# Optimization experiments

Hardware: AMD Instinct MI355X
Metric: run time of the kernel (lower is better)

The kernel has to match this reference:

```python
import jax, jax.numpy as jnp
import numpy as np

D = 128      # dim_hidden
L = 8        # topological levels (level 0 = primary inputs)
M = 32768    # nodes per level
N = L * M
G = 5        # gate types: maj/not/and/or/xor -> 5 param sets
F = 2        # fan-in per gate node


def setup_inputs() -> dict:
    key = jax.random.key(0)
    ks = jax.random.split(key, 18)
    p = lambda k, sh: jax.random.normal(k, sh, jnp.float32) * 0.05
    return {
        's': jax.random.normal(ks[0], (N, D), jnp.float32),
        't': jax.random.normal(ks[1], (N, D), jnp.float32),
        'gate': jax.random.randint(ks[2], (N,), 0, G, jnp.int32),
        'fanin': jax.random.randint(ks[3], (L - 1, M, F), 0, M, jnp.int32),
        'hs_W': p(ks[4], (2 * D, D)), 'hs_b': p(ks[5], (D,)),
        'aggr_W1': p(ks[6], (G, 2 * D, D)), 'aggr_b1': p(ks[7], (G, D)),
        'aggr_W2': p(ks[8], (G, D, D)), 'aggr_b2': p(ks[9], (G, D)),
        'aggr_W3': p(ks[10], (G, D, D)), 'aggr_b3': p(ks[11], (G, D)),
        'gru_Wi': p(ks[12], (G, D, 3 * D)), 'gru_Wh': p(ks[13], (G, D, 3 * D)),
        'gru_bi': p(ks[14], (G, 3 * D)), 'gru_bh': p(ks[15], (G, 3 * D)),
    }


def _forward(s, t, gate, fanin, hs_W, hs_b, aggr_W1, aggr_b1, aggr_W2, aggr_b2,
             aggr_W3, aggr_b3, gru_Wi, gru_Wh, gru_bi, gru_bh):
    hs = jnp.concatenate([s, t], -1) @ hs_W + hs_b          # [N,D]
    hf = jnp.zeros((N, D), hs.dtype)                        # functional state, zero-init
    for lvl in range(1, L):                                 # level-synchronous sweep
        lo = lvl * M
        g_l = gate[lo:lo + M]                               # [M] gate type of dst nodes
        oh = jax.nn.one_hot(g_l, G, dtype=hs.dtype)         # [M,G] gate selector
        src = (lvl - 1) * M + fanin[lvl - 1]                # [M,F] global fan-in indices
        src_state = jnp.concatenate([hs[src], hf[src]], -1)  # [M,F,2D] node_state gather
        # per-gate-type edge MLP (TFMlpAggr): 3-layer MLP on source states, sum over fan-in
        h1 = jax.nn.relu(jnp.einsum('mfc,gcd->gmfd', src_state, aggr_W1) + aggr_b1[:, None, None, :])
        h2 = jax.nn.relu(jnp.einsum('gmfd,gde->gmfe', h1, aggr_W2) + aggr_b2[:, None, None, :])
        m = jnp.einsum('gmfe,gek->gmfk', h2, aggr_W3) + aggr_b3[:, None, None, :]
        msg = jnp.einsum('gmd,mg->md', m.sum(axis=2), oh)   # [M,D] select own gate's aggr
        # per-gate-type GRU update of hf (torch GRU math, seq_len=1)
        h = hf[lo:lo + M]                                   # [M,D]
        gi = jnp.einsum('md,gdk->gmk', msg, gru_Wi) + gru_bi[:, None, :]  # [G,M,3D]
        gh = jnp.einsum('md,gdk->gmk', h, gru_Wh) + gru_bh[:, None, :]
        r = jax.nn.sigmoid(gi[..., :D] + gh[..., :D])
        z = jax.nn.sigmoid(gi[..., D:2 * D] + gh[..., D:2 * D])
        n = jnp.tanh(gi[..., 2 * D:] + r * gh[..., 2 * D:])
        h_new = jnp.einsum('gmd,mg->md', (1.0 - z) * n + z * h[None], oh)
        hf = hf.at[lo:lo + M].set(h_new)                    # scatter-write back
    return hs, hf


def reference(s, t, gate, fanin, hs_W, hs_b, aggr_W1, aggr_b1, aggr_W2, aggr_b2,
              aggr_W3, aggr_b3, gru_Wi, gru_Wh, gru_bi, gru_bh):
    return _forward(s, t, gate, fanin, hs_W, hs_b, aggr_W1, aggr_b1, aggr_W2,
                    aggr_b2, aggr_W3, aggr_b3, gru_Wi, gru_Wh, gru_bi, gru_bh)
```

## Files before the change

### kernel.cpp

```cpp
#include <hip/hip_runtime.h>
#include <hip/hip_bf16.h>

#define DD 128
#define LL 8
#define MM 32768
#define NN (LL*MM)
#define GG 5
#define FF 2
#define SORT_STRIDE 33408

typedef __attribute__((ext_vector_type(8))) short short8;
typedef __attribute__((ext_vector_type(4))) short short4v;
typedef __attribute__((ext_vector_type(4))) float f32x4;

#define MFMA16(a,b,c) __builtin_amdgcn_mfma_f32_16x16x32_bf16((a),(b),(c),0,0,0)

__device__ __forceinline__ short f2bf(float x){
  __hip_bfloat16 h = __float2bfloat16(x);
  return *reinterpret_cast<short*>(&h);
}

__device__ __forceinline__ short8 pack8(f32x4 a, f32x4 b){
  short8 r;
  r[0]=f2bf(a[0]); r[1]=f2bf(a[1]); r[2]=f2bf(a[2]); r[3]=f2bf(a[3]);
  r[4]=f2bf(b[0]); r[5]=f2bf(b[1]); r[6]=f2bf(b[2]); r[7]=f2bf(b[3]);
  return r;
}

__global__ void prep_kernel(const float* __restrict__ hs_W, const float* __restrict__ W1,
                            const float* __restrict__ W2, const float* __restrict__ W3,
                            const float* __restrict__ Wi,
                            short* __restrict__ hsWt, short* __restrict__ W1t,
                            short* __restrict__ W2t, short* __restrict__ W3t,
                            short* __restrict__ Wit, int* __restrict__ cntcur)
{
  if (blockIdx.x == 0 && threadIdx.x < 70) cntcur[threadIdx.x] = 0;
  int u = blockIdx.x*256 + threadIdx.x;
  const float* src; short* dst; int ldw;
  if (u < 4096){
    int i=u, ct=i>>9, kc=(i>>6)&7, ln=i&63;
    src = hs_W + (size_t)(kc*32 + 8*(ln>>4))*128 + ct*16 + (ln&15);
    dst = hsWt + (size_t)i*8; ldw=128;
  } else if (u < 24576){
    int v=u-4096, g=v>>12, i=v&4095, ct=i>>9, kc=(i>>6)&7, ln=i&63;
    src = W1 + (size_t)g*32768 + (size_t)(kc*32 + 8*(ln>>4))*128 + ct*16 + (ln&15);
    dst = W1t + (size_t)g*32768 + i*8; ldw=128;
  } else if (u < 34816){
    int v=u-24576, g=v>>11, i=v&2047, ct=i>>8, kc=(i>>6)&3, ln=i&63;
    src = W2 + (size_t)g*16384 + (size_t)(kc*32 + 8*(ln>>4))*128 + ct*16 + (ln&15);
    dst = W2t + (size_t)g*16384 + i*8; ldw=128;
  } else if (u < 45056){
    int v=u-34816, g=v>>11, i=v&2047, ct=i>>8, kc=(i>>6)&3, ln=i&63;
    src = W3 + (size_t)g*16384 + (size_t)(kc*32 + 8*(ln>>4))*128 + ct*16 + (ln&15);
    dst = W3t + (size_t)g*16384 + i*8; ldw=128;
  } else {
    int v=u-45056, g=v/6144, i=v%6144, ct=i>>8, kc=(i>>6)&3, ln=i&63;
    src = Wi + (size_t)g*49152 + (size_t)(kc*32 + 8*(ln>>4))*384 + ct*16 + (ln&15);
    dst = Wit + (size_t)g*49152 + i*8; ldw=384;
  }
  short8 o;
#pragma unroll
  for (int j=0;j<8;++j) o[j] = f2bf(src[(size_t)j*ldw]);
  *(short8*)dst = o;
}

__global__ void count_kernel(const int* __restrict__ gate, int* __restrict__ cnt){
  __shared__ int lc[GG];
  const int li = blockIdx.x >> 7;
  const int m  = ((blockIdx.x & 127) << 8) + threadIdx.x;
  if (threadIdx.x < GG) lc[threadIdx.x] = 0;
  __syncthreads();
  int g = gate[(li+1)*MM + m];
  atomicAdd(&lc[g], 1);
  __syncthreads();
  if (threadIdx.x < GG && lc[threadIdx.x] > 0)
    atomicAdd(&cnt[li*GG + threadIdx.x], lc[threadIdx.x]);
}

__global__ void offs_kernel(const int* __restrict__ cnt, int* __restrict__ off,
                            int* __restrict__ pend, int* __restrict__ sorted){
  __shared__ int se[35], sp[35];
  const int tid = threadIdx.x;
  if (tid < LL-1){
    int l = tid, o = 0;
    for (int g = 0; g < GG; ++g){
      off[l*GG+g] = o;
      int c = cnt[l*GG+g];
      pend[l*GG+g] = o + c;
      se[l*GG+g] = o + c;
      o += ((c + 31) >> 5) << 5;
      sp[l*GG+g] = o;
    }
  }
  __syncthreads();
  for (int b = 0; b < 35; ++b){
    int l = b / GG;
    for (int i = se[b] + tid; i < sp[b]; i += 256)
      sorted[l*SORT_STRIDE + i] = -1;
  }
}

__global__ void scatter_kernel(const int* __restrict__ gate, const int* __restrict__ off,
                               int* __restrict__ cur, int* __restrict__ sorted){
  __shared__ int lc[GG];
  __shared__ int base[GG];
  const int li = blockIdx.x >> 7;
  const int m  = ((blockIdx.x & 127) << 8) + threadIdx.x;
  if (threadIdx.x < GG) lc[threadIdx.x] = 0;
  __syncthreads();
  int g = gate[(li+1)*MM + m];
  int p = atomicAdd(&lc[g], 1);
  __syncthreads();
  if (threadIdx.x < GG)
    base[threadIdx.x] = atomicAdd(&cur[li*GG + threadIdx.x], lc[threadIdx.x]);
  __syncthreads();
  sorted[li*SORT_STRIDE + off[li*GG+g] + base[g] + p] = m;
}

__global__ __launch_bounds__(256,3) void hs_kernel(
    const float* __restrict__ s, const float* __restrict__ t,
    const short* __restrict__ Wt, const float* __restrict__ b,
    float* __restrict__ hs, short* __restrict__ hs_sh,
    float* __restrict__ hf, short* __restrict__ hf_sh)
{
  __shared__ __align__(16) short Xs[16384];
  const int tid=threadIdx.x, lane=tid&63, w=tid>>6;
  const int l15=lane&15, lq=lane>>4;
  const int row0 = blockIdx.x*64;

  {
    const int r = tid>>2, p = tid&3;
    const float* srow = s + (size_t)(row0+r)*DD;
    const float* trow = t + (size_t)(row0+r)*DD;
    const int rf = r>>4, rl = r&15;
    f32x4 va[16];
#pragma unroll
    for (int i=0;i<8;++i){
      int u = p + 4*i;
      const float* pp = (u<16) ? (srow + 8*u) : (trow + 8*(u-16));
      va[2*i]   = *(const f32x4*)pp;
      va[2*i+1] = *(const f32x4*)(pp+4);
    }
#pragma unroll
    for (int i=0;i<8;++i){
      int u = p + 4*i;
      short8 v = pack8(va[2*i], va[2*i+1]);
      *(short8*)(Xs + ((rf*8+(u>>2))*64 + (u&3)*16 + rl)*8) = v;
    }
  }

  if (row0 < MM){
    f32x4 zf4 = {0.f,0.f,0.f,0.f};
    short8 zs8 = {0,0,0,0,0,0,0,0};
    const size_t basei = (size_t)row0*DD;
    for (int i=tid; i<2048; i+=256) *(f32x4*)(hf + basei + i*4) = zf4;
    for (int i=tid; i<1024; i+=256) *(short8*)(hf_sh + basei + i*8) = zs8;
  }
  __syncthreads();

  f32x4 zf = {0.f,0.f,0.f,0.f};
  const short* Aw = Wt + (16*w)*512 + lane*8;
  short8 af[16];
#pragma unroll
  for (int i=0;i<16;++i) af[i] = *(const short8*)(Aw + i*512);

  f32x4 acc[4][2];
#pragma unroll
  for (int rr=0;rr<4;++rr){ acc[rr][0]=zf; acc[rr][1]=zf; }
#pragma unroll
  for (int kc=0;kc<8;++kc){
    short8 bx[4];
#pragma unroll
    for (int rr=0;rr<4;++rr)
      bx[rr] = *(const short8*)(Xs + ((rr*8 + kc)*64 + lane)*8);
#pragma unroll
    for (int rr=0;rr<4;++rr){
      acc[rr][0] = MFMA16(af[kc],   bx[rr], acc[rr][0]);
      acc[rr][1] = MFMA16(af[8+kc], bx[rr], acc[rr][1]);
    }
  }

  f32x4 bv0 = *(const f32x4*)(b + 32*w + 4*lq);
  f32x4 bv1 = *(const f32x4*)(b + 32*w + 16 + 4*lq);
#pragma unroll
  for (int rr=0;rr<4;++rr){
    int row = row0 + rr*16 + l15;
#pragma unroll
    for (int q=0;q<2;++q){
      f32x4 bv = q ? bv1 : bv0;
      int col = 32*w + 16*q + 4*lq;
      f32x4 o; short4v pk;
#pragma unroll
      for (int j=0;j<4;++j){ o[j] = acc[rr][q][j] + bv[j]; pk[j] = f2bf(o[j]); }
      *(f32x4*)(hs + (size_t)row*DD + col) = o;
      *(short4v*)(hs_sh + (size_t)row*DD + col) = pk;
    }
  }
}

__global__ __launch_bounds__(256,3) void level_kernel(
    int lvl, float* __restrict__ hfg,
    const short* __restrict__ hs_sh, short* __restrict__ hf_sh,
    const int* __restrict__ fanin,
    const short* __restrict__ W1t, const short* __restrict__ W2t,
    const short* __restrict__ W3t, const short* __restrict__ Wit,
    const float* __restrict__ b1, const float* __restrict__ b2,
    const float* __restrict__ b3, const float* __restrict__ bi,
    const float* __restrict__ bh,
    const int* __restrict__ off, const int* __restrict__ pend,
    const int* __restrict__ sorted)
{
  __shared__ __align__(16) short Xs[16384];
  __shared__ int nodebuf[32];
  __shared__ int srcbuf[64];
  __shared__ int ginfo;

  const int tid=threadIdx.x, lane=tid&63, w=tid>>6;
  const int l15=lane&15, lq=lane>>4;
  const int li = lvl-1;
  const int pos0 = blockIdx.x*32;

  if (tid==0){
    int g=-1;
    for (int q=0;q<GG;++q)
      if (pos0>=off[li*GG+q] && pos0<pend[li*GG+q]){ g=q; break; }
    ginfo=g;
  }
  if (tid<32) nodebuf[tid] = sorted[li*SORT_STRIDE + pos0 + tid];
  if (tid<64){
    int mg = sorted[li*SORT_STRIDE + pos0 + (tid>>1)];
    srcbuf[tid] = (mg>=0) ? li*MM + fanin[((size_t)li*MM+mg)*FF + (tid&1)] : 0;
  }
  __syncthreads();
  const int g = ginfo;
  if (g<0) return;

  {
    const int r = tid>>2, p = tid&3;
    const int src = srcbuf[r];
    const short* hsrow = hs_sh + (size_t)src*DD;
    const short* hfrow = hf_sh + (size_t)src*DD;
    const int rf = r>>4, rl = r&15;
    short8 va[8];
#pragma unroll
    for (int i=0;i<8;++i){
      int u = p + 4*i;
      va[i] = *(const short8*)((u<16) ? (hsrow + 8*u) : (hfrow + 8*(u-16)));
    }
#pragma unroll
    for (int i=0;i<8;++i){
      int u = p + 4*i;
      *(short8*)(Xs + ((rf*8+(u>>2))*64 + (u&3)*16 + rl)*8) = va[i];
    }
  }
  __syncthreads();

  f32x4 zf = {0.f,0.f,0.f,0.f};

  f32x4 acc[4][2];
#pragma unroll
  for (int rr=0;rr<4;++rr){ acc[rr][0]=zf; acc[rr][1]=zf; }
  {
    const short* A1w = W1t + (size_t)g*32768 + (16*w)*512 + lane*8;
    short8 af[16];
#pragma unroll
    for (int i=0;i<16;++i) af[i] = *(const short8*)(A1w + i*512);
#pragma unroll
    for (int kc=0;kc<8;++kc){
      short8 bx[4];
#pragma unroll
      for (int rr=0;rr<4;++rr)
        bx[rr] = *(const short8*)(Xs + ((rr*8 + kc)*64 + lane)*8);
#pragma unroll
      for (int rr=0;rr<4;++rr){
        acc[rr][0] = MFMA16(af[kc],   bx[rr], acc[rr][0]);
        acc[rr][1] = MFMA16(af[8+kc], bx[rr], acc[rr][1]);
      }
    }
  }
  __syncthreads();
  {
    f32x4 bv0 = *(const f32x4*)(b1 + g*DD + 32*w + 4*lq);
    f32x4 bv1 = *(const f32x4*)(b1 + g*DD + 32*w + 16 + 4*lq);
#pragma unroll
    for (int rr=0;rr<4;++rr){
#pragma unroll
      for (int q=0;q<2;++q){
        f32x4 bv = q ? bv1 : bv0;
        short4v pk;
#pragma unroll
        for (int j=0;j<4;++j) pk[j] = f2bf(fmaxf(acc[rr][q][j] + bv[j], 0.f));
        *(short4v*)(Xs + ((rr*4 + w)*64 + (2*q + (lq>>1))*16 + l15)*8 + 4*(lq&1)) = pk;
      }
    }
  }
  __syncthreads();

  f32x4 acc2[4][2];
#pragma unroll
  for (int rr=0;rr<4;++rr){ acc2[rr][0]=zf; acc2[rr][1]=zf; }
  {
    const short* A2w = W2t + (size_t)g*16384 + (8*w)*512 + lane*8;
    short8 af[8];
#pragma unroll
    for (int i=0;i<8;++i) af[i] = *(const short8*)(A2w + i*512);
#pragma unroll
    for (int kc=0;kc<4;++kc){
      short8 bx[4];
#pragma unroll
      for (int rr=0;rr<4;++rr)
        bx[rr] = *(const short8*)(Xs + ((rr*4 + kc)*64 + lane)*8);
#pragma unroll
      for (int rr=0;rr<4;++rr){
        acc2[rr][0] = MFMA16(af[kc],   bx[rr], acc2[rr][0]);
        acc2[rr][1] = MFMA16(af[4+kc], bx[rr], acc2[rr][1]);
      }
    }
  }
  {
    f32x4 bv0 = *(const f32x4*)(b2 + g*DD + 32*w + 4*lq);
    f32x4 bv1 = *(const f32x4*)(b2 + g*DD + 32*w + 16 + 4*lq);
#pragma unroll
    for (int rr=0;rr<4;++rr){
#pragma unroll
      for (int q=0;q<2;++q){
        f32x4 bv = q ? bv1 : bv0;
        short4v pk;
#pragma unroll
        for (int j=0;j<4;++j) pk[j] = f2bf(fmaxf(acc2[rr][q][j] + bv[j], 0.f));
        *(short4v*)(Xs + 8192 + ((rr*4 + w)*64 + (2*q + (lq>>1))*16 + l15)*8 + 4*(lq&1)) = pk;
      }
    }
  }
  __syncthreads();

  f32x4 acc3[4][2];
#pragma unroll
  for (int rr=0;rr<4;++rr){ acc3[rr][0]=zf; acc3[rr][1]=zf; }
  {
    const short* A3w = W3t + (size_t)g*16384 + (8*w)*512 + lane*8;
    short8 af[8];
#pragma unroll
    for (int i=0;i<8;++i) af[i] = *(const short8*)(A3w + i*512);
#pragma unroll
    for (int kc=0;kc<4;++kc){
      short8 bx[4];
#pragma unroll
      for (int rr=0;rr<4;++rr)
        bx[rr] = *(const short8*)(Xs + 8192 + ((rr*4 + kc)*64 + lane)*8);
#pragma unroll
      for (int rr=0;rr<4;++rr){
        acc3[rr][0] = MFMA16(af[kc],   bx[rr], acc3[rr][0]);
        acc3[rr][1] = MFMA16(af[4+kc], bx[rr], acc3[rr][1]);
      }
    }
  }
  {
    f32x4 bv0 = *(const f32x4*)(b3 + g*DD + 32*w + 4*lq);
    f32x4 bv1 = *(const f32x4*)(b3 + g*DD + 32*w + 16 + 4*lq);
#pragma unroll
    for (int rr=0;rr<4;++rr){
#pragma unroll
      for (int q=0;q<2;++q){
        f32x4 bv = q ? bv1 : bv0;
        f32x4 mv;
#pragma unroll
        for (int j=0;j<4;++j){
          float v = acc3[rr][q][j];
          mv[j] = v + __shfl_xor(v, 1) + 2.f*bv[j];
        }
        if ((l15 & 1) == 0){
          int n = rr*8 + (l15>>1);
          short4v pk;
#pragma unroll
          for (int j=0;j<4;++j) pk[j] = f2bf(mv[j]);
          *(short4v*)(Xs + (((n>>4)*4 + w)*64 + (2*q + (lq>>1))*16 + (n&15))*8 + 4*(lq&1)) = pk;
        }
      }
    }
  }
  __syncthreads();

  const short* AW = Wit + (size_t)g*49152 + lane*8;
  const int lo = lvl*MM;
#pragma unroll
  for (int q=0;q<2;++q){
    short8 af[12];
#pragma unroll
    for (int kc=0;kc<4;++kc){
      int cti = ((2*w + q)*4 + kc)*512;
      af[kc]   = *(const short8*)(AW + cti);
      af[4+kc] = *(const short8*)(AW + 16384 + cti);
      af[8+kc] = *(const short8*)(AW + 32768 + cti);
    }
    f32x4 gr[2], gz[2], gn[2];
    gr[0]=zf; gr[1]=zf; gz[0]=zf; gz[1]=zf; gn[0]=zf; gn[1]=zf;
#pragma unroll
    for (int kc=0;kc<4;++kc){
#pragma unroll
      for (int rfm=0;rfm<2;++rfm){
        short8 bm = *(const short8*)(Xs + ((rfm*4 + kc)*64 + lane)*8);
        gr[rfm] = MFMA16(af[kc],   bm, gr[rfm]);
        gz[rfm] = MFMA16(af[4+kc], bm, gz[rfm]);
        gn[rfm] = MFMA16(af[8+kc], bm, gn[rfm]);
      }
    }
    int col = 32*w + 16*q + 4*lq;
    f32x4 biR = *(const f32x4*)(bi + g*384 + col);
    f32x4 biZ = *(const f32x4*)(bi + g*384 + 128 + col);
    f32x4 biN = *(const f32x4*)(bi + g*384 + 256 + col);
    f32x4 bhR = *(const f32x4*)(bh + g*384 + col);
    f32x4 bhZ = *(const f32x4*)(bh + g*384 + 128 + col);
    f32x4 bhN = *(const f32x4*)(bh + g*384 + 256 + col);
#pragma unroll
    for (int rfm=0;rfm<2;++rfm){
      int m = nodebuf[rfm*16 + l15];
      if (m < 0) continue;
      f32x4 o; short4v pk;
#pragma unroll
      for (int j=0;j<4;++j){
        float xr = gr[rfm][j] + biR[j] + bhR[j];
        float xz = gz[rfm][j] + biZ[j] + bhZ[j];
        float r_ = 1.f/(1.f + __expf(-xr));
        float z_ = 1.f/(1.f + __expf(-xz));
        float xn = gn[rfm][j] + biN[j] + r_*bhN[j];
        float n_ = 2.f/(1.f + __expf(-2.f*xn)) - 1.f;
        o[j] = (1.f - z_)*n_;
        pk[j] = f2bf(o[j]);
      }
      *(f32x4*)(hfg + (size_t)(lo + m)*DD + col) = o;
      *(short4v*)(hf_sh + (size_t)(lo + m)*DD + col) = pk;
    }
  }
}

extern "C" void kernel_launch(void* const* d_in, const int* in_sizes, int n_in,
                              void* d_out, int out_size, void* d_ws, size_t ws_size,
                              hipStream_t stream)
{
  const float* s    = (const float*)d_in[0];
  const float* t    = (const float*)d_in[1];
  const int*   gate = (const int*)d_in[2];
  const int*   fanin= (const int*)d_in[3];
  const float* hs_W = (const float*)d_in[4];
  const float* hs_b = (const float*)d_in[5];
  const float* W1   = (const float*)d_in[6];
  const float* b1   = (const float*)d_in[7];
  const float* W2   = (const float*)d_in[8];
  const float* b2   = (const float*)d_in[9];
  const float* W3   = (const float*)d_in[10];
  const float* b3   = (const float*)d_in[11];
  const float* Wi   = (const float*)d_in[12];
  const float* bi   = (const float*)d_in[14];
  const float* bh   = (const float*)d_in[15];

  float* hs = (float*)d_out;
  float* hf = hs + (size_t)NN*DD;

  int* cnt    = (int*)d_ws;
  int* cur    = cnt + 35;
  int* off    = cnt + 70;
  int* pendv  = cnt + 105;
  int* sorted = cnt + 256;

  short* wbase = (short*)((char*)d_ws + (1<<20));
  short* hsWt = wbase;
  short* W1t  = wbase + 32768;
  short* W2t  = wbase + 196608;
  short* W3t  = wbase + 278528;
  short* Wit  = wbase + 360448;

  short* hs_sh = (short*)((char*)d_ws + (size_t)(8<<20));
  short* hf_sh = hs_sh + (size_t)NN*DD;

  prep_kernel<<<296, 256, 0, stream>>>(hs_W, W1, W2, W3, Wi,
                                       hsWt, W1t, W2t, W3t, Wit, cnt);
  count_kernel<<<896, 256, 0, stream>>>(gate, cnt);
  offs_kernel<<<1, 256, 0, stream>>>(cnt, off, pendv, sorted);
  scatter_kernel<<<896, 256, 0, stream>>>(gate, off, cur, sorted);
  hs_kernel<<<NN/64, 256, 0, stream>>>(s, t, hsWt, hs_b, hs, hs_sh, hf, hf_sh);
  for (int lvl = 1; lvl < LL; ++lvl){
    level_kernel<<<SORT_STRIDE/32, 256, 0, stream>>>(lvl, hf,
        hs_sh, hf_sh, fanin, W1t, W2t, W3t, Wit,
        b1, b2, b3, bi, bh, off, pendv, sorted);
  }
}
```

Baseline: 403.2 us.

## Raise occupancy bounds, add nontemporal memory ops, drop shared-memory index prologue

Launch bounds for hs_kernel and level_kernel go from 3 to 5 waves per SIMD, which forces tighter register use. Input reads and the fp32 output writes now use nontemporal loads and stores, and explicit vmcnt(0) waits are placed after the global-load batches. The level kernel no longer stages gate, node and source indices in shared memory behind a barrier; each thread computes them itself with redundant global loads. The tighter register cap risks spills given the large fragment arrays held per thread, and the hard waits may serialize memory latency.

```diff
diff --git a/kernel.cpp b/kernel.cpp
--- a/kernel.cpp
+++ b/kernel.cpp
@@ -14,6 +14,7 @@
 typedef __attribute__((ext_vector_type(4))) float f32x4;
 
 #define MFMA16(a,b,c) __builtin_amdgcn_mfma_f32_16x16x32_bf16((a),(b),(c),0,0,0)
+#define VMEM_FENCE() asm volatile("s_waitcnt vmcnt(0)" ::: "memory")
 
 __device__ __forceinline__ short f2bf(float x){
   __hip_bfloat16 h = __float2bfloat16(x);
@@ -117,7 +118,7 @@
   sorted[li*SORT_STRIDE + off[li*GG+g] + base[g] + p] = m;
 }
 
-__global__ __launch_bounds__(256,3) void hs_kernel(
+__global__ __launch_bounds__(256,5) void hs_kernel(
     const float* __restrict__ s, const float* __restrict__ t,
     const short* __restrict__ Wt, const float* __restrict__ b,
     float* __restrict__ hs, short* __restrict__ hs_sh,
@@ -138,9 +139,10 @@
     for (int i=0;i<8;++i){
       int u = p + 4*i;
       const float* pp = (u<16) ? (srow + 8*u) : (trow + 8*(u-16));
-      va[2*i]   = *(const f32x4*)pp;
-      va[2*i+1] = *(const f32x4*)(pp+4);
-    }
+      va[2*i]   = __builtin_nontemporal_load((const f32x4*)pp);
+      va[2*i+1] = __builtin_nontemporal_load((const f32x4*)(pp+4));
+    }
+    VMEM_FENCE();
 #pragma unroll
     for (int i=0;i<8;++i){
       int u = p + 4*i;
@@ -153,7 +155,8 @@
     f32x4 zf4 = {0.f,0.f,0.f,0.f};
     short8 zs8 = {0,0,0,0,0,0,0,0};
     const size_t basei = (size_t)row0*DD;
-    for (int i=tid; i<2048; i+=256) *(f32x4*)(hf + basei + i*4) = zf4;
+    for (int i=tid; i<2048; i+=256)
+      __builtin_nontemporal_store(zf4, (f32x4*)(hf + basei + i*4));
     for (int i=tid; i<1024; i+=256) *(short8*)(hf_sh + basei + i*8) = zs8;
   }
   __syncthreads();
@@ -163,6 +166,7 @@
   short8 af[16];
 #pragma unroll
   for (int i=0;i<16;++i) af[i] = *(const short8*)(Aw + i*512);
+  VMEM_FENCE();
 
   f32x4 acc[4][2];
 #pragma unroll
@@ -192,13 +196,13 @@
       f32x4 o; short4v pk;
 #pragma unroll
       for (int j=0;j<4;++j){ o[j] = acc[rr][q][j] + bv[j]; pk[j] = f2bf(o[j]); }
-      *(f32x4*)(hs + (size_t)row*DD + col) = o;
+      __builtin_nontemporal_store(o, (f32x4*)(hs + (size_t)row*DD + col));
       *(short4v*)(hs_sh + (size_t)row*DD + col) = pk;
     }
   }
 }
 
-__global__ __launch_bounds__(256,3) void level_kernel(
+__global__ __launch_bounds__(256,5) void level_kernel(
     int lvl, float* __restrict__ hfg,
     const short* __restrict__ hs_sh, short* __restrict__ hf_sh,
     const int* __restrict__ fanin,
@@ -211,33 +215,21 @@
     const int* __restrict__ sorted)
 {
   __shared__ __align__(16) short Xs[16384];
-  __shared__ int nodebuf[32];
-  __shared__ int srcbuf[64];
-  __shared__ int ginfo;
-
   const int tid=threadIdx.x, lane=tid&63, w=tid>>6;
   const int l15=lane&15, lq=lane>>4;
   const int li = lvl-1;
   const int pos0 = blockIdx.x*32;
 
-  if (tid==0){
-    int g=-1;
-    for (int q=0;q<GG;++q)
-      if (pos0>=off[li*GG+q] && pos0<pend[li*GG+q]){ g=q; break; }
-    ginfo=g;
-  }
-  if (tid<32) nodebuf[tid] = sorted[li*SORT_STRIDE + pos0 + tid];
-  if (tid<64){
-    int mg = sorted[li*SORT_STRIDE + pos0 + (tid>>1)];
-    srcbuf[tid] = (mg>=0) ? li*MM + fanin[((size_t)li*MM+mg)*FF + (tid&1)] : 0;
-  }
-  __syncthreads();
-  const int g = ginfo;
-  if (g<0) return;
+  int g = -1;
+#pragma unroll
+  for (int q=0;q<GG;++q)
+    if (pos0 >= off[li*GG+q] && pos0 < pend[li*GG+q]) g = q;
+  if (g < 0) return;
 
   {
     const int r = tid>>2, p = tid&3;
-    const int src = srcbuf[r];
+    const int mg = sorted[li*SORT_STRIDE + pos0 + (r>>1)];
+    const int src = (mg>=0) ? li*MM + fanin[((size_t)li*MM+mg)*FF + (r&1)] : 0;
     const short* hsrow = hs_sh + (size_t)src*DD;
     const short* hfrow = hf_sh + (size_t)src*DD;
     const int rf = r>>4, rl = r&15;
@@ -247,6 +239,7 @@
       int u = p + 4*i;
       va[i] = *(const short8*)((u<16) ? (hsrow + 8*u) : (hfrow + 8*(u-16)));
     }
+    VMEM_FENCE();
 #pragma unroll
     for (int i=0;i<8;++i){
       int u = p + 4*i;
@@ -265,6 +258,7 @@
     short8 af[16];
 #pragma unroll
     for (int i=0;i<16;++i) af[i] = *(const short8*)(A1w + i*512);
+    VMEM_FENCE();
 #pragma unroll
     for (int kc=0;kc<8;++kc){
       short8 bx[4];
@@ -304,6 +298,7 @@
     short8 af[8];
 #pragma unroll
     for (int i=0;i<8;++i) af[i] = *(const short8*)(A2w + i*512);
+    VMEM_FENCE();
 #pragma unroll
     for (int kc=0;kc<4;++kc){
       short8 bx[4];
@@ -342,6 +337,7 @@
     short8 af[8];
 #pragma unroll
     for (int i=0;i<8;++i) af[i] = *(const short8*)(A3w + i*512);
+    VMEM_FENCE();
 #pragma unroll
     for (int kc=0;kc<4;++kc){
       short8 bx[4];
@@ -383,6 +379,8 @@
 
   const short* AW = Wit + (size_t)g*49152 + lane*8;
   const int lo = lvl*MM;
+  const int m0 = sorted[li*SORT_STRIDE + pos0 + l15];
+  const int m1 = sorted[li*SORT_STRIDE + pos0 + 16 + l15];
 #pragma unroll
   for (int q=0;q<2;++q){
     short8 af[12];
@@ -393,6 +391,7 @@
       af[4+kc] = *(const short8*)(AW + 16384 + cti);
       af[8+kc] = *(const short8*)(AW + 32768 + cti);
     }
+    VMEM_FENCE();
     f32x4 gr[2], gz[2], gn[2];
     gr[0]=zf; gr[1]=zf; gz[0]=zf; gz[1]=zf; gn[0]=zf; gn[1]=zf;
 #pragma unroll
@@ -414,7 +413,7 @@
     f32x4 bhN = *(const f32x4*)(bh + g*384 + 256 + col);
 #pragma unroll
     for (int rfm=0;rfm<2;++rfm){
-      int m = nodebuf[rfm*16 + l15];
+      int m = rfm ? m1 : m0;
       if (m < 0) continue;
       f32x4 o; short4v pk;
 #pragma unroll
@@ -428,7 +427,7 @@
         o[j] = (1.f - z_)*n_;
         pk[j] = f2bf(o[j]);
       }
-      *(f32x4*)(hfg + (size_t)(lo + m)*DD + col) = o;
+      __builtin_nontemporal_store(o, (f32x4*)(hfg + (size_t)(lo + m)*DD + col));
       *(short4v*)(hf_sh + (size_t)(lo + m)*DD + col) = pk;
     }
   }
```

New measurement: 388.2 us. -3.7%, faster.
